# Kernel tuning notes

Hardware: AMD Instinct MI355X
Metric: run time of the kernel (lower is better)

Reference implementation:

```python
import jax, jax.numpy as jnp
import numpy as np

VOCAB, EMB, NDIM, B, T = 50000, 300, 512, 128, 128


def gru_cell(x, h, Wih, Whh, bih, bhh):
    # torch nn.GRU gate order: [r, z, n]
    gi = x @ Wih.T + bih
    gh = h @ Whh.T + bhh
    i_r, i_z, i_n = jnp.split(gi, 3, axis=-1)
    h_r, h_z, h_n = jnp.split(gh, 3, axis=-1)
    r = jax.nn.sigmoid(i_r + h_r)
    z = jax.nn.sigmoid(i_z + h_z)
    n = jnp.tanh(i_n + r * h_n)
    return (1.0 - z) * n + z * h


def masked_gru(X, mask, h0, Wih, Whh, bih, bhh):
    # X: T x B x d, mask: T x B, h0: B x n. Replicates _gru_forward:
    # step-0 output is stored UNmasked (o_tm1 is None), later steps blend.
    h_raw = gru_cell(X[0], h0, Wih, Whh, bih, bhh)
    m0 = mask[0][:, None]
    h = h_raw * m0 + h0 * (1.0 - m0)
    o = h_raw

    def step(carry, inp):
        h, o = carry
        x_t, m_t = inp
        m = m_t[:, None]
        hr = gru_cell(x_t, h, Wih, Whh, bih, bhh)
        h_new = hr * m + h * (1.0 - m)
        o_new = hr * m + o * (1.0 - m)
        return (h_new, o_new), o_new

    (h_f, _), o_rest = jax.lax.scan(step, (h, o), (X[1:], mask[1:]))
    return jnp.concatenate([o[None], o_rest], axis=0), h_f


def rte_forward(premise, hypothesis, E, p_Wih, p_Whh, p_bih, p_bhh,
                h_Wih, h_Whh, h_bih, h_bhh, m_Wih, m_Whh, m_bih, m_bhh,
                W_y, W_h, W_r, W_alpha, out_W, out_b):
    bsz = premise.shape[0]
    n_dim = W_y.shape[0]
    mask_p = (premise != 0).astype(E.dtype).T            # T x B
    mask_h = (hypothesis != 0).astype(E.dtype).T
    enc_p = E[premise].transpose(1, 0, 2)                # T x B x EMB (eval: no dropout)
    enc_h = E[hypothesis].transpose(1, 0, 2)
    h0 = jnp.zeros((bsz, n_dim), dtype=E.dtype)
    o_p, h_n = masked_gru(enc_p, mask_p, h0, p_Wih, p_Whh, p_bih, p_bhh)
    o_h, _ = masked_gru(enc_h, mask_h, h_n, h_Wih, h_Whh, h_bih, h_bhh)

    Y = o_p.transpose(1, 0, 2)                           # B x Tp x n
    Yw = Y @ W_y                                         # hoisted: constant across steps
    maskY = mask_p.T                                     # B x Tp

    def step(r, inp):
        h_t, m_t = inp
        s = h_t @ W_h + r @ W_r                          # B x n
        M = jnp.tanh(Yw + s[:, None, :])                 # B x Tp x n
        alpha = (M @ W_alpha)[..., 0]                    # B x Tp
        alpha = alpha - 1000.0 * (1.0 - maskY)
        alpha = jax.nn.softmax(alpha, axis=-1)
        a = jnp.einsum('bt,btn->bn', alpha, Y)
        m_in = jnp.concatenate([a, h_t], axis=-1)        # B x 2n
        rr = gru_cell(m_in, r, m_Wih, m_Whh, m_bih, m_bhh)
        m = m_t[:, None]
        r_new = rr * m + r * (1.0 - m)
        return r_new, alpha

    r0 = jnp.zeros((bsz, n_dim), dtype=E.dtype)
    r_f, _alpha_vec = jax.lax.scan(step, r0, (o_h, mask_h))
    logits = r_f @ out_W.T + out_b                       # B x 3
    return jax.nn.log_softmax(logits, axis=-1)


def setup_inputs():
    key = jax.random.key(0)
    ks = jax.random.split(key, 22)
    s = 0.05
    def rn(k, sh):
        return jax.random.normal(k, sh, dtype=jnp.float32) * s
    G = 3 * NDIM
    return {
        "premise": jax.random.randint(ks[0], (B, T), 0, VOCAB),
        "hypothesis": jax.random.randint(ks[1], (B, T), 0, VOCAB),
        "E": rn(ks[2], (VOCAB, EMB)),
        "p_Wih": rn(ks[3], (G, EMB)), "p_Whh": rn(ks[4], (G, NDIM)),
        "p_bih": rn(ks[5], (G,)), "p_bhh": rn(ks[6], (G,)),
        "h_Wih": rn(ks[7], (G, EMB)), "h_Whh": rn(ks[8], (G, NDIM)),
        "h_bih": rn(ks[9], (G,)), "h_bhh": rn(ks[10], (G,)),
        "m_Wih": rn(ks[11], (G, 2 * NDIM)), "m_Whh": rn(ks[12], (G, NDIM)),
        "m_bih": rn(ks[13], (G,)), "m_bhh": rn(ks[14], (G,)),
        "W_y": rn(ks[15], (NDIM, NDIM)), "W_h": rn(ks[16], (NDIM, NDIM)),
        "W_r": rn(ks[17], (NDIM, NDIM)), "W_alpha": rn(ks[18], (NDIM, 1)),
        "out_W": rn(ks[19], (3, NDIM)), "out_b": rn(ks[20], (3,)),
    }


def reference(premise, hypothesis, E, p_Wih, p_Whh, p_bih, p_bhh,
              h_Wih, h_Whh, h_bih, h_bhh, m_Wih, m_Whh, m_bih, m_bhh,
              W_y, W_h, W_r, W_alpha, out_W, out_b):
    return rte_forward(premise, hypothesis, E, p_Wih, p_Whh, p_bih, p_bhh,
                       h_Wih, h_Whh, h_bih, h_bhh, m_Wih, m_Whh, m_bih, m_bhh,
                       W_y, W_h, W_r, W_alpha, out_W, out_b)
```

## Files before the change

kernel.cpp:

```cpp
#include <hip/hip_runtime.h>
#include <math.h>

#define B_SZ 128
#define T_SZ 128
#define EMBD 300
#define ND 512
#define G3 1536
#define FPAD 32
#define NFID 128
#define NREP 8

typedef short s16x8 __attribute__((ext_vector_type(8)));
typedef float f32x4 __attribute__((ext_vector_type(4)));
typedef unsigned long long u64;

__device__ __forceinline__ unsigned short f2b(float x) {
    unsigned u = __float_as_uint(x);
    unsigned r = (u + 0x7fff + ((u >> 16) & 1)) >> 16;
    return (unsigned short)r;
}
__device__ __forceinline__ float b2f(unsigned short v) {
    return __uint_as_float(((unsigned)v) << 16);
}
__device__ __forceinline__ float fsigmoid(float x) { return 1.0f / (1.0f + __expf(-x)); }
__device__ __forceinline__ float ftanh(float x) { return 1.0f - 2.0f / (__expf(2.0f * x) + 1.0f); }

__device__ __forceinline__ f32x4 mfma16(s16x8 a, s16x8 b, f32x4 c) {
    return __builtin_amdgcn_mfma_f32_16x16x32_bf16(a, b, c, 0, 0, 0);
}

__device__ __forceinline__ u64 cld64(const void* p) {
    return __hip_atomic_load((const u64*)p, __ATOMIC_RELAXED, __HIP_MEMORY_SCOPE_AGENT);
}
__device__ __forceinline__ void cst64(void* p, u64 v) {
    __hip_atomic_store((u64*)p, v, __ATOMIC_RELAXED, __HIP_MEMORY_SCOPE_AGENT);
}
__device__ __forceinline__ unsigned cld32(const void* p) {
    return __hip_atomic_load((const unsigned*)p, __ATOMIC_RELAXED, __HIP_MEMORY_SCOPE_AGENT);
}
__device__ __forceinline__ void cst32(void* p, unsigned v) {
    __hip_atomic_store((unsigned*)p, v, __ATOMIC_RELAXED, __HIP_MEMORY_SCOPE_AGENT);
}
__device__ __forceinline__ s16x8 cld_frag(const unsigned short* p) {
    union { u64 q[2]; s16x8 v; } u;
    u.q[0] = cld64(p);
    u.q[1] = cld64(p + 4);
    return u.v;
}

__device__ __forceinline__ void postflag(unsigned* flags, int base, int id, unsigned ep)
{
    if (threadIdx.x < NREP)
        cst32(&flags[((long)threadIdx.x * NFID + base + id) * FPAD], ep);
}
__device__ __forceinline__ void waitflags(const unsigned* flags, int base, int n,
                                          unsigned ep, int rep)
{
    const unsigned* fr = flags + (long)rep * NFID * FPAD;
    if (threadIdx.x < 64) {
#pragma unroll 1
        for (int i = threadIdx.x; i < n; i += 64)
            while (cld32(&fr[(long)(base + i) * FPAD]) < ep)
                __builtin_amdgcn_s_sleep(2);
    }
    __syncthreads();
}
__device__ __forceinline__ void fbar(unsigned* flags, int base, int nb, unsigned ep)
{
    __syncthreads();
    postflag(flags, base, blockIdx.x & 63, ep);
    waitflags(flags, base, nb, ep, blockIdx.x & 7);
}

#define FB_GRUP 0
#define FB_GRUH 64

template<typename AT, bool OB>
__global__ __launch_bounds__(256)
void mfma_gemm(const AT* __restrict__ A, const int* __restrict__ idxA,
               const unsigned short* __restrict__ Wb, const float* __restrict__ bias,
               void* __restrict__ Cv,
               int M, int N, int K, int ldA, int Kpad, int ldC)
{
    __shared__ unsigned short As[64][40];
    __shared__ unsigned short Bs[64][40];
    const int tid = threadIdx.x;
    const int wv = tid >> 6, lane = tid & 63;
    const int wm = wv >> 1, wn = wv & 1;
    const int m0 = blockIdx.y * 64, n0 = blockIdx.x * 64;

    f32x4 acc[2][2] = {{{0.f,0.f,0.f,0.f},{0.f,0.f,0.f,0.f}},
                       {{0.f,0.f,0.f,0.f},{0.f,0.f,0.f,0.f}}};
    const int r_st = tid >> 2, k_st = (tid & 3) * 8;

    long arow = -1;
    {
        int gm = m0 + r_st;
        if (gm < M) arow = idxA ? (long)idxA[gm] : (long)gm;
    }

    const int kIters = (K + 31) / 32;
    for (int it = 0; it < kIters; ++it) {
        const int kg = it * 32 + k_st;
        {
            s16x8 pk = {0,0,0,0,0,0,0,0};
            if (arow >= 0) {
                if constexpr (sizeof(AT) == 2) {
                    if (kg + 8 <= K) {
                        pk = *(const s16x8*)((const unsigned short*)A + arow * (long)ldA + kg);
                    } else {
#pragma unroll
                        for (int j = 0; j < 8; ++j)
                            if (kg + j < K) pk[j] = (short)((const unsigned short*)A)[arow * (long)ldA + kg + j];
                    }
                } else {
                    if (kg + 8 <= K) {
                        const float* p = (const float*)A + arow * (long)ldA + kg;
                        f32x4 u0 = *(const f32x4*)p;
                        f32x4 u1 = *(const f32x4*)(p + 4);
#pragma unroll
                        for (int j = 0; j < 4; ++j) { pk[j] = (short)f2b(u0[j]); pk[4+j] = (short)f2b(u1[j]); }
                    } else {
#pragma unroll
                        for (int j = 0; j < 8; ++j) {
                            int kk = kg + j;
                            if (kk < K) pk[j] = (short)f2b(((const float*)A)[arow * (long)ldA + kk]);
                        }
                    }
                }
            }
            *(s16x8*)&As[r_st][k_st] = pk;
        }
        {
            int gn = n0 + r_st;
            s16x8 pk = {0,0,0,0,0,0,0,0};
            if (gn < N) pk = *(const s16x8*)&Wb[(long)gn * Kpad + kg];
            *(s16x8*)&Bs[r_st][k_st] = pk;
        }
        __syncthreads();
        {
            const int koff = (lane >> 4) * 8;
            s16x8 af[2], bfr[2];
#pragma unroll
            for (int f = 0; f < 2; ++f) {
                af[f]  = *(s16x8*)&As[wm * 32 + f * 16 + (lane & 15)][koff];
                bfr[f] = *(s16x8*)&Bs[wn * 32 + f * 16 + (lane & 15)][koff];
            }
#pragma unroll
            for (int fi = 0; fi < 2; ++fi)
#pragma unroll
                for (int fj = 0; fj < 2; ++fj)
                    acc[fi][fj] = mfma16(af[fi], bfr[fj], acc[fi][fj]);
        }
        __syncthreads();
    }
#pragma unroll
    for (int fi = 0; fi < 2; ++fi)
#pragma unroll
        for (int fj = 0; fj < 2; ++fj)
#pragma unroll
            for (int r = 0; r < 4; ++r) {
                int m = m0 + wm * 32 + fi * 16 + (lane >> 4) * 4 + r;
                int n = n0 + wn * 32 + fj * 16 + (lane & 15);
                if (m < M && n < N) {
                    float v = acc[fi][fj][r];
                    if (bias) v += bias[n];
                    if constexpr (OB) ((unsigned short*)Cv)[(long)m * ldC + n] = f2b(v);
                    else               ((float*)Cv)[(long)m * ldC + n] = v;
                }
            }
}

#define GRU_NB 64
__global__ __launch_bounds__(256, 1)
void gru_chain(const unsigned short* __restrict__ Whh_b, const float* __restrict__ GI,
               const float* __restrict__ bhh, const int* __restrict__ toks,
               float* __restrict__ h32,
               unsigned short* __restrict__ h16a, unsigned short* __restrict__ h16b,
               unsigned short* __restrict__ o_bt,
               unsigned* __restrict__ flags, int fbase)
{
    __shared__ unsigned short wlds[3][16][512];
    __shared__ unsigned short ht[64][20];
    const int tid = threadIdx.x;
    const int wv = tid >> 6, lane = tid & 63;
    const int dt = blockIdx.x & 31, bh = blockIdx.x >> 5;
    const int b0 = bh * 64;

    for (int s = 0; s < 12; ++s) {
        int slot = tid + s * 256;
        int g = slot >> 10, rem = slot & 1023, ks = rem >> 6, ln = rem & 63;
        int row = g * ND + dt * 16 + (ln & 15);
        int k = ks * 32 + (ln >> 4) * 8;
        *(s16x8*)&wlds[g][ks][ln * 8] = *(const s16x8*)&Whh_b[(long)row * ND + k];
    }
    __syncthreads();

    const int d = dt * 16 + (lane & 15);
    const int brow = b0 + wv * 16 + (lane >> 4) * 4;
    const long fhrd = ((long)(bh * 4 + wv) * 16) << 9;

    const int bl = tid & 63, dq = tid >> 6;
    const long fhwr = (((long)(bh * 4 + (bl >> 4)) * 16 + (dt >> 1)) << 9)
                    + (((((dt & 1) * 16 + dq * 4) >> 3) * 16 + (bl & 15)) * 8)
                    + (((dt & 1) * 16 + dq * 4) & 7);

    float hreg[4];
#pragma unroll
    for (int rr = 0; rr < 4; ++rr) hreg[rr] = h32[(long)(brow + rr) * ND + d];

    float o_run[4] = {0.f, 0.f, 0.f, 0.f};
    unsigned ep = 0;

    for (int t = 0; t < T_SZ; ++t) {
        const unsigned short* hin16 = (t & 1) ? h16b : h16a;
        unsigned short* hout16 = (t & 1) ? h16a : h16b;

        const float* git = GI + (long)t * (B_SZ * G3);
        float gi_r[4], gi_z[4], gi_n[4]; int mk[4];
#pragma unroll
        for (int rr = 0; rr < 4; ++rr) {
            int b = brow + rr;
            gi_r[rr] = git[(long)b * G3 + d];
            gi_z[rr] = git[(long)b * G3 + ND + d];
            gi_n[rr] = git[(long)b * G3 + 2 * ND + d];
            mk[rr]   = toks[b * T_SZ + t];
        }

        f32x4 acc0 = {0,0,0,0}, acc1 = {0,0,0,0}, acc2 = {0,0,0,0};
#pragma unroll
        for (int ks = 0; ks < 16; ++ks) {
            s16x8 a  = cld_frag(&hin16[fhrd + ((long)ks << 9) + lane * 8]);
            s16x8 br = *(s16x8*)&wlds[0][ks][lane * 8];
            s16x8 bz = *(s16x8*)&wlds[1][ks][lane * 8];
            s16x8 bn = *(s16x8*)&wlds[2][ks][lane * 8];
            acc0 = mfma16(a, br, acc0);
            acc1 = mfma16(a, bz, acc1);
            acc2 = mfma16(a, bn, acc2);
        }

#pragma unroll
        for (int rr = 0; rr < 4; ++rr) {
            int b = brow + rr;
            float rg = fsigmoid(gi_r[rr] + acc0[rr] + bhh[d]);
            float zg = fsigmoid(gi_z[rr] + acc1[rr] + bhh[ND + d]);
            float ng = ftanh(gi_n[rr] + rg * (acc2[rr] + bhh[2 * ND + d]));
            float hr = (1.0f - zg) * ng + zg * hreg[rr];
            bool m = mk[rr] != 0;
            float hn = m ? hr : hreg[rr];
            hreg[rr] = hn;
            ht[b - b0][lane & 15] = f2b(hn);
            if (t == T_SZ - 1) h32[(long)b * ND + d] = hn;
            o_run[rr] = (t == 0) ? hr : (m ? hr : o_run[rr]);
            o_bt[((long)b * T_SZ + t) * ND + d] = f2b(o_run[rr]);
        }
        __syncthreads();
        {
            u64 v = *(u64*)&ht[bl][dq * 4];
            cst64(&hout16[fhwr], v);
        }
        fbar(flags, fbase, GRU_NB, ++ep);
    }
}

__global__ __launch_bounds__(512, 1)
void match_pb(const unsigned short* __restrict__ Ws,
              const unsigned short* __restrict__ Wg,
              const unsigned short* __restrict__ OHWh_bt,
              const unsigned short* __restrict__ OHGI_bt,
              const float* __restrict__ m_bhh, const float* __restrict__ Walpha,
              const unsigned short* __restrict__ Yw_bb,
              const unsigned short* __restrict__ Y_bb,
              const int* __restrict__ prem, const int* __restrict__ hyp,
              float* __restrict__ r32)
{
    __shared__ unsigned short ylds[T_SZ][ND];
    __shared__ float xv[1024];
    __shared__ float sarr[512];
    __shared__ float wal[512];
    __shared__ float part[512];
    __shared__ float lg[T_SZ];

    const int b = blockIdx.x;
    const int tid = threadIdx.x;
    const int tp = tid >> 2, q = tid & 3;

    for (int s = 0; s < 16; ++s) {
        int c = s * 512 + tid;
        int row = c >> 6, cg = c & 63;
        *(s16x8*)&ylds[row][cg * 8] =
            *(const s16x8*)&Y_bb[((long)b * T_SZ + row) * ND + cg * 8];
    }
    s16x8 ywr[16];
#pragma unroll
    for (int i8 = 0; i8 < 16; ++i8)
        ywr[i8] = *(const s16x8*)&Yw_bb[((long)b * T_SZ + tp) * ND + q * 128 + i8 * 8];

    wal[tid] = Walpha[tid];
    xv[512 + tid] = 0.0f;
    float mm = 0.f;
    if (tid < T_SZ) mm = (prem[b * T_SZ + tid] != 0) ? 0.f : 1000.f;
    __syncthreads();

    const float* sp  = &sarr[q * 128];
    const float* wap = &wal[q * 128];

    for (int t = 0; t < T_SZ; ++t) {
        {
            float acc = 0.f;
            const unsigned short* wp = Ws + (long)tid * 8;
#pragma unroll 4
            for (int k8 = 0; k8 < 64; ++k8) {
                f32x4 x0 = *(const f32x4*)&xv[512 + k8 * 8];
                f32x4 x1 = *(const f32x4*)&xv[512 + k8 * 8 + 4];
                s16x8 w = *(const s16x8*)(wp + ((long)k8 << 12));
#pragma unroll
                for (int j = 0; j < 4; ++j) {
                    acc += b2f((unsigned short)w[j]) * x0[j];
                    acc += b2f((unsigned short)w[4 + j]) * x1[j];
                }
            }
            sarr[tid] = acc + b2f(OHWh_bt[((long)b * T_SZ + t) * ND + tid]);
        }
        __syncthreads();
        {
            float acc = 0.f;
#pragma unroll
            for (int i8 = 0; i8 < 16; ++i8) {
                s16x8 yw = ywr[i8];
                f32x4 s0 = *(const f32x4*)&sp[i8 * 8];
                f32x4 s1 = *(const f32x4*)&sp[i8 * 8 + 4];
                f32x4 w0 = *(const f32x4*)&wap[i8 * 8];
                f32x4 w1 = *(const f32x4*)&wap[i8 * 8 + 4];
#pragma unroll
                for (int j = 0; j < 4; ++j)
                    acc += ftanh(b2f((unsigned short)yw[j]) + s0[j]) * w0[j];
#pragma unroll
                for (int j = 0; j < 4; ++j)
                    acc += ftanh(b2f((unsigned short)yw[4 + j]) + s1[j]) * w1[j];
            }
            part[tid] = acc;
        }
        __syncthreads();
        if (tid < T_SZ)
            lg[tid] = __expf(part[tid * 4] + part[tid * 4 + 1]
                           + part[tid * 4 + 2] + part[tid * 4 + 3] - mm);
        __syncthreads();
        {
            float suml = 0.f, av = 0.f;
#pragma unroll 8
            for (int tpp = 0; tpp < T_SZ; ++tpp) {
                float al = lg[tpp];
                suml += al;
                av += al * b2f(ylds[tpp][tid]);
            }
            xv[tid] = av / suml;
        }
        __syncthreads();
        {
            float aR = 0.f, aZ = 0.f, aGN = 0.f, aHN = 0.f;
            const unsigned short* wb = Wg + (long)tid * 8;
#pragma unroll 2
            for (int k8 = 0; k8 < 64; ++k8) {
                f32x4 xa0 = *(const f32x4*)&xv[k8 * 8];
                f32x4 xa1 = *(const f32x4*)&xv[k8 * 8 + 4];
                f32x4 xr0 = *(const f32x4*)&xv[512 + k8 * 8];
                f32x4 xr1 = *(const f32x4*)&xv[512 + k8 * 8 + 4];
                const long ko = (long)k8 << 12;
                s16x8 wRa = *(const s16x8*)(wb + ko);
                s16x8 wZa = *(const s16x8*)(wb + ko + (1L << 18));
                s16x8 wNa = *(const s16x8*)(wb + ko + (2L << 18));
                s16x8 wRr = *(const s16x8*)(wb + ko + (3L << 18));
                s16x8 wZr = *(const s16x8*)(wb + ko + (4L << 18));
                s16x8 wNr = *(const s16x8*)(wb + ko + (5L << 18));
#pragma unroll
                for (int j = 0; j < 4; ++j) {
                    aR  += b2f((unsigned short)wRa[j]) * xa0[j];
                    aR  += b2f((unsigned short)wRa[4 + j]) * xa1[j];
                    aZ  += b2f((unsigned short)wZa[j]) * xa0[j];
                    aZ  += b2f((unsigned short)wZa[4 + j]) * xa1[j];
                    aGN += b2f((unsigned short)wNa[j]) * xa0[j];
                    aGN += b2f((unsigned short)wNa[4 + j]) * xa1[j];
                    aR  += b2f((unsigned short)wRr[j]) * xr0[j];
                    aR  += b2f((unsigned short)wRr[4 + j]) * xr1[j];
                    aZ  += b2f((unsigned short)wZr[j]) * xr0[j];
                    aZ  += b2f((unsigned short)wZr[4 + j]) * xr1[j];
                    aHN += b2f((unsigned short)wNr[j]) * xr0[j];
                    aHN += b2f((unsigned short)wNr[4 + j]) * xr1[j];
                }
            }
            const unsigned short* og = OHGI_bt + ((long)b * T_SZ + t) * G3;
            float rg = fsigmoid(aR + b2f(og[tid]) + m_bhh[tid]);
            float zg = fsigmoid(aZ + b2f(og[ND + tid]) + m_bhh[ND + tid]);
            float ng = ftanh(aGN + b2f(og[2 * ND + tid])
                             + rg * (aHN + m_bhh[2 * ND + tid]));
            float rp = xv[512 + tid];
            float rn = (1.0f - zg) * ng + zg * rp;
            bool mk = hyp[b * T_SZ + t] != 0;
            float v = mk ? rn : rp;
            __syncthreads();
            xv[512 + tid] = v;
        }
        __syncthreads();
    }
    r32[(long)b * ND + tid] = xv[512 + tid];
}

__global__ void prep_idx(const int* __restrict__ prem, const int* __restrict__ hyp,
                         int* __restrict__ idx_p, int* __restrict__ idx_h)
{
    int i = blockIdx.x * blockDim.x + threadIdx.x;
    if (i < B_SZ * T_SZ) {
        int t = i / B_SZ, b = i % B_SZ;
        idx_p[i] = prem[b * T_SZ + t];
        idx_h[i] = hyp[b * T_SZ + t];
    }
}

__global__ void conv_w(const float* __restrict__ in, unsigned short* __restrict__ out,
                       int N, int K, int Kpad, int ldIn, int colOff)
{
    long i = (long)blockIdx.x * blockDim.x + threadIdx.x;
    if (i >= (long)N * Kpad) return;
    int n = (int)(i / Kpad), k = (int)(i % Kpad);
    float v = (k < K) ? in[(long)n * ldIn + k + colOff] : 0.0f;
    out[i] = f2b(v);
}

__global__ void conv_wT(const float* __restrict__ in, unsigned short* __restrict__ out,
                        int N, int K, int Kpad, int ldIn)
{
    long i = (long)blockIdx.x * blockDim.x + threadIdx.x;
    if (i >= (long)N * Kpad) return;
    int n = (int)(i / Kpad), k = (int)(i % Kpad);
    float v = (k < K) ? in[(long)k * ldIn + n] : 0.0f;
    out[i] = f2b(v);
}

__global__ void pack_ws(const float* __restrict__ Wr, unsigned short* __restrict__ out)
{
    long i = (long)blockIdx.x * blockDim.x + threadIdx.x;
    if (i >= 64L * 512 * 8) return;
    int k8 = (int)(i >> 12), n = (int)((i >> 3) & 511), j = (int)(i & 7);
    out[i] = f2b(Wr[(long)(k8 * 8 + j) * ND + n]);
}

__global__ void pack_wg(const float* __restrict__ mWih, const float* __restrict__ mWhh,
                        unsigned short* __restrict__ out)
{
    long i = (long)blockIdx.x * blockDim.x + threadIdx.x;
    if (i >= 6L * 64 * 512 * 8) return;
    int fam = (int)(i >> 18);
    long rem = i & 262143;
    int k8 = (int)(rem >> 12), n = (int)((rem >> 3) & 511), j = (int)(rem & 7);
    int k = k8 * 8 + j;
    float v;
    if (fam < 3) v = mWih[(long)(fam * ND + n) * 1024 + k];
    else         v = mWhh[(long)((fam - 3) * ND + n) * ND + k];
    out[i] = f2b(v);
}

__global__ void zero_kernel(float* __restrict__ p, int n)
{
    int i = blockIdx.x * blockDim.x + threadIdx.x;
    if (i < n) p[i] = 0.0f;
}

__global__ void final_logits(const float* __restrict__ r, const float* __restrict__ outW,
                             const float* __restrict__ outb, float* __restrict__ out)
{
    int b = blockIdx.x;
    int lane = threadIdx.x;
    float a0 = 0.0f, a1 = 0.0f, a2 = 0.0f;
    for (int k = lane; k < ND; k += 64) {
        float rv = r[(long)b * ND + k];
        a0 += rv * outW[0 * ND + k];
        a1 += rv * outW[1 * ND + k];
        a2 += rv * outW[2 * ND + k];
    }
#pragma unroll
    for (int off = 32; off; off >>= 1) {
        a0 += __shfl_down(a0, off);
        a1 += __shfl_down(a1, off);
        a2 += __shfl_down(a2, off);
    }
    if (lane == 0) {
        float l0 = a0 + outb[0], l1 = a1 + outb[1], l2 = a2 + outb[2];
        float mx = fmaxf(l0, fmaxf(l1, l2));
        float se = expf(l0 - mx) + expf(l1 - mx) + expf(l2 - mx);
        float ls = mx + logf(se);
        out[b * 3 + 0] = l0 - ls;
        out[b * 3 + 1] = l1 - ls;
        out[b * 3 + 2] = l2 - ls;
    }
}

extern "C" void kernel_launch(void* const* d_in, const int* in_sizes, int n_in,
                              void* d_out, int out_size, void* d_ws, size_t ws_size,
                              hipStream_t stream)
{
    const int*   prem    = (const int*)d_in[0];
    const int*   hyp     = (const int*)d_in[1];
    const float* E       = (const float*)d_in[2];
    const float* p_Wih   = (const float*)d_in[3];
    const float* p_Whh   = (const float*)d_in[4];
    const float* p_bih   = (const float*)d_in[5];
    const float* p_bhh   = (const float*)d_in[6];
    const float* h_Wih   = (const float*)d_in[7];
    const float* h_Whh   = (const float*)d_in[8];
    const float* h_bih   = (const float*)d_in[9];
    const float* h_bhh   = (const float*)d_in[10];
    const float* m_Wih   = (const float*)d_in[11];
    const float* m_Whh   = (const float*)d_in[12];
    const float* m_bih   = (const float*)d_in[13];
    const float* m_bhh   = (const float*)d_in[14];
    const float* W_y     = (const float*)d_in[15];
    const float* W_h     = (const float*)d_in[16];
    const float* W_r     = (const float*)d_in[17];
    const float* W_alpha = (const float*)d_in[18];
    const float* out_W   = (const float*)d_in[19];
    const float* out_b   = (const float*)d_in[20];
    float* out = (float*)d_out;

    const int MB = T_SZ * B_SZ;
    const int NFLAGS = NREP * NFID * FPAD;

    float* ws = (float*)d_ws;
    size_t off = 0;
    float* GI    = ws + off; off += (size_t)MB * G3;
    float* h32   = ws + off; off += (size_t)B_SZ * ND;
    float* r32   = ws + off; off += (size_t)B_SZ * ND;
    unsigned* flags = (unsigned*)(ws + off); off += NFLAGS;
    int* idx_p = (int*)(ws + off); off += (size_t)B_SZ * T_SZ;
    int* idx_h = (int*)(ws + off); off += (size_t)B_SZ * T_SZ;
    unsigned short* ub = (unsigned short*)(ws + off);
    size_t uoff = 0;
    unsigned short* o_p_bt = ub + uoff; uoff += (size_t)MB * ND;
    unsigned short* o_h_bt = ub + uoff; uoff += (size_t)MB * ND;
    unsigned short* Yw_bb  = ub + uoff; uoff += (size_t)MB * ND;
    unsigned short* OHWh_bt= ub + uoff; uoff += (size_t)MB * ND;
    unsigned short* OHGI_bt= ub + uoff; uoff += (size_t)MB * G3;
    unsigned short* h16a   = ub + uoff; uoff += (size_t)B_SZ * ND;
    unsigned short* h16b   = ub + uoff; uoff += (size_t)B_SZ * ND;
    unsigned short* pWih_b = ub + uoff; uoff += (size_t)G3 * 320;
    unsigned short* hWih_b = ub + uoff; uoff += (size_t)G3 * 320;
    unsigned short* pWhh_b = ub + uoff; uoff += (size_t)G3 * ND;
    unsigned short* hWhh_b = ub + uoff; uoff += (size_t)G3 * ND;
    unsigned short* mWihR  = ub + uoff; uoff += (size_t)G3 * ND;
    unsigned short* WyT_b  = ub + uoff; uoff += (size_t)ND * ND;
    unsigned short* WhT_b  = ub + uoff; uoff += (size_t)ND * ND;
    unsigned short* Ws_p   = ub + uoff; uoff += 64L * 512 * 8;
    unsigned short* Wg_p   = ub + uoff; uoff += 6L * 64 * 512 * 8;
    off += (uoff + 1) / 2;
    if (ws_size < off * sizeof(float)) return;

    auto cblk = [](long n) { return (int)((n + 255) / 256); };

    prep_idx<<<cblk(MB), 256, 0, stream>>>(prem, hyp, idx_p, idx_h);
    conv_w <<<cblk((long)G3 * 320), 256, 0, stream>>>(p_Wih, pWih_b, G3, EMBD, 320, EMBD, 0);
    conv_w <<<cblk((long)G3 * 320), 256, 0, stream>>>(h_Wih, hWih_b, G3, EMBD, 320, EMBD, 0);
    conv_w <<<cblk((long)G3 * ND), 256, 0, stream>>>(p_Whh, pWhh_b, G3, ND, ND, ND, 0);
    conv_w <<<cblk((long)G3 * ND), 256, 0, stream>>>(h_Whh, hWhh_b, G3, ND, ND, ND, 0);
    conv_w <<<cblk((long)G3 * ND), 256, 0, stream>>>(m_Wih, mWihR, G3, ND, ND, 2 * ND, ND);
    conv_wT<<<cblk((long)ND * ND), 256, 0, stream>>>(W_y, WyT_b, ND, ND, ND, ND);
    conv_wT<<<cblk((long)ND * ND), 256, 0, stream>>>(W_h, WhT_b, ND, ND, ND, ND);
    pack_ws<<<cblk(64L * 512 * 8), 256, 0, stream>>>(W_r, Ws_p);
    pack_wg<<<cblk(6L * 64 * 512 * 8), 256, 0, stream>>>(m_Wih, m_Whh, Wg_p);
    zero_kernel<<<cblk(B_SZ * ND), 256, 0, stream>>>(h32, B_SZ * ND);
    zero_kernel<<<cblk(B_SZ * ND / 2), 256, 0, stream>>>((float*)h16a, B_SZ * ND / 2);
    zero_kernel<<<cblk(NFLAGS), 256, 0, stream>>>((float*)flags, NFLAGS);

    {
        dim3 g(G3 / 64, MB / 64);
        mfma_gemm<float, false><<<g, 256, 0, stream>>>(E, idx_p, pWih_b, p_bih, GI,
                                                       MB, G3, EMBD, EMBD, 320, G3);
    }
    gru_chain<<<GRU_NB, 256, 0, stream>>>(pWhh_b, GI, p_bhh, prem, h32, h16a, h16b,
                                          o_p_bt, flags, FB_GRUP);

    {
        dim3 g(G3 / 64, MB / 64);
        mfma_gemm<float, false><<<g, 256, 0, stream>>>(E, idx_h, hWih_b, h_bih, GI,
                                                       MB, G3, EMBD, EMBD, 320, G3);
    }
    gru_chain<<<GRU_NB, 256, 0, stream>>>(hWhh_b, GI, h_bhh, hyp, h32, h16a, h16b,
                                          o_h_bt, flags, FB_GRUH);

    {
        dim3 g(ND / 64, MB / 64);
        mfma_gemm<unsigned short, true><<<g, 256, 0, stream>>>(o_p_bt, nullptr, WyT_b, nullptr,
                                                               Yw_bb, MB, ND, ND, ND, ND, ND);
        mfma_gemm<unsigned short, true><<<g, 256, 0, stream>>>(o_h_bt, nullptr, WhT_b, nullptr,
                                                               OHWh_bt, MB, ND, ND, ND, ND, ND);
        dim3 g2(G3 / 64, MB / 64);
        mfma_gemm<unsigned short, true><<<g2, 256, 0, stream>>>(o_h_bt, nullptr, mWihR, m_bih,
                                                                OHGI_bt, MB, G3, ND, ND, ND, G3);
    }

    match_pb<<<B_SZ, 512, 0, stream>>>(Ws_p, Wg_p, OHWh_bt, OHGI_bt, m_bhh, W_alpha,
                                       Yw_bb, o_p_bt, prem, hyp, r32);

    final_logits<<<B_SZ, 64, 0, stream>>>(r32, out_W, out_b, out);
}
```

Baseline: 7.689 ms.

## Use packed bf16 v_dot2 in match kernel with bf16-packed activations

Rewrites the match_pb recurrence to use v_dot2_f32_bf16 for the Ws and Wg matvecs and for the attention-weighted sum over Y. Activations (attention context, recurrent state, softmax weights) are packed to bf16 pairs in shared memory, and Y is stored as interleaved time-pairs so each dot2 covers two timesteps. This halves the multiply-add instruction count and removes per-element bf16-to-float unpacking, but adds extra pack steps and barriers per timestep and rounds activations and softmax weights to bf16, which loses precision.

```diff
diff --git a/kernel.cpp b/kernel.cpp
--- a/kernel.cpp
+++ b/kernel.cpp
@@ -22,8 +22,16 @@
 __device__ __forceinline__ float b2f(unsigned short v) {
     return __uint_as_float(((unsigned)v) << 16);
 }
+__device__ __forceinline__ unsigned pk2(float lo, float hi) {
+    return (unsigned)f2b(lo) | ((unsigned)f2b(hi) << 16);
+}
 __device__ __forceinline__ float fsigmoid(float x) { return 1.0f / (1.0f + __expf(-x)); }
 __device__ __forceinline__ float ftanh(float x) { return 1.0f - 2.0f / (__expf(2.0f * x) + 1.0f); }
+
+__device__ __forceinline__ float dot2bf(unsigned a, unsigned b, float c) {
+    asm("v_dot2_f32_bf16 %0, %1, %2, %0" : "+v"(c) : "v"(a), "v"(b));
+    return c;
+}
 
 __device__ __forceinline__ f32x4 mfma16(s16x8 a, s16x8 b, f32x4 c) {
     return __builtin_amdgcn_mfma_f32_16x16x32_bf16(a, b, c, 0, 0, 0);
@@ -274,22 +282,29 @@
               const int* __restrict__ prem, const int* __restrict__ hyp,
               float* __restrict__ r32)
 {
-    __shared__ unsigned short ylds[T_SZ][ND];
-    __shared__ float xv[1024];
+    __shared__ unsigned ytp[64][512];
     __shared__ float sarr[512];
     __shared__ float wal[512];
     __shared__ float part[512];
     __shared__ float lg[T_SZ];
+    __shared__ unsigned lgp[64];
+    __shared__ unsigned xa16[256];
+    __shared__ unsigned xr16[256];
+    __shared__ float xr32[512];
 
     const int b = blockIdx.x;
     const int tid = threadIdx.x;
     const int tp = tid >> 2, q = tid & 3;
 
-    for (int s = 0; s < 16; ++s) {
-        int c = s * 512 + tid;
-        int row = c >> 6, cg = c & 63;
-        *(s16x8*)&ylds[row][cg * 8] =
-            *(const s16x8*)&Y_bb[((long)b * T_SZ + row) * ND + cg * 8];
+    for (int s = 0; s < 8; ++s) {
+        int idx = s * 512 + tid;
+        int rp = idx >> 6, n0 = (idx & 63) * 8;
+        s16x8 y0 = *(const s16x8*)&Y_bb[((long)b * T_SZ + 2 * rp) * ND + n0];
+        s16x8 y1 = *(const s16x8*)&Y_bb[((long)b * T_SZ + 2 * rp + 1) * ND + n0];
+#pragma unroll
+        for (int j = 0; j < 8; ++j)
+            ytp[rp][n0 + j] = (unsigned)(unsigned short)y0[j]
+                            | ((unsigned)(unsigned short)y1[j] << 16);
     }
     s16x8 ywr[16];
 #pragma unroll
@@ -297,28 +312,30 @@
         ywr[i8] = *(const s16x8*)&Yw_bb[((long)b * T_SZ + tp) * ND + q * 128 + i8 * 8];
 
     wal[tid] = Walpha[tid];
-    xv[512 + tid] = 0.0f;
+    xr32[tid] = 0.0f;
+    if (tid < 256) xr16[tid] = 0u;
     float mm = 0.f;
     if (tid < T_SZ) mm = (prem[b * T_SZ + tid] != 0) ? 0.f : 1000.f;
     __syncthreads();
 
     const float* sp  = &sarr[q * 128];
     const float* wap = &wal[q * 128];
+    const unsigned* wsp = (const unsigned*)Ws + tid * 4;
+    const unsigned* wgp = (const unsigned*)Wg + tid * 4;
+    const unsigned ONE2 = 0x3F803F80u;
 
     for (int t = 0; t < T_SZ; ++t) {
         {
             float acc = 0.f;
-            const unsigned short* wp = Ws + (long)tid * 8;
 #pragma unroll 4
             for (int k8 = 0; k8 < 64; ++k8) {
-                f32x4 x0 = *(const f32x4*)&xv[512 + k8 * 8];
-                f32x4 x1 = *(const f32x4*)&xv[512 + k8 * 8 + 4];
-                s16x8 w = *(const s16x8*)(wp + ((long)k8 << 12));
-#pragma unroll
-                for (int j = 0; j < 4; ++j) {
-                    acc += b2f((unsigned short)w[j]) * x0[j];
-                    acc += b2f((unsigned short)w[4 + j]) * x1[j];
-                }
+                unsigned x0 = xr16[k8 * 4], x1 = xr16[k8 * 4 + 1];
+                unsigned x2 = xr16[k8 * 4 + 2], x3 = xr16[k8 * 4 + 3];
+                const unsigned* w = wsp + (long)k8 * 2048;
+                acc = dot2bf(w[0], x0, acc);
+                acc = dot2bf(w[1], x1, acc);
+                acc = dot2bf(w[2], x2, acc);
+                acc = dot2bf(w[3], x3, acc);
             }
             sarr[tid] = acc + b2f(OHWh_bt[((long)b * T_SZ + t) * ND + tid]);
         }
@@ -346,64 +363,67 @@
             lg[tid] = __expf(part[tid * 4] + part[tid * 4 + 1]
                            + part[tid * 4 + 2] + part[tid * 4 + 3] - mm);
         __syncthreads();
-        {
-            float suml = 0.f, av = 0.f;
+        if (tid < 64) lgp[tid] = pk2(lg[2 * tid], lg[2 * tid + 1]);
+        __syncthreads();
+        {
+            float av = 0.f, su = 0.f;
 #pragma unroll 8
-            for (int tpp = 0; tpp < T_SZ; ++tpp) {
-                float al = lg[tpp];
-                suml += al;
-                av += al * b2f(ylds[tpp][tid]);
+            for (int i = 0; i < 64; ++i) {
+                unsigned l2 = lgp[i];
+                unsigned y2 = ytp[i][tid];
+                av = dot2bf(l2, y2, av);
+                su = dot2bf(l2, ONE2, su);
             }
-            xv[tid] = av / suml;
-        }
+            part[tid] = av / su;
+        }
+        __syncthreads();
+        if (tid < 256) xa16[tid] = pk2(part[2 * tid], part[2 * tid + 1]);
         __syncthreads();
         {
             float aR = 0.f, aZ = 0.f, aGN = 0.f, aHN = 0.f;
-            const unsigned short* wb = Wg + (long)tid * 8;
 #pragma unroll 2
             for (int k8 = 0; k8 < 64; ++k8) {
-                f32x4 xa0 = *(const f32x4*)&xv[k8 * 8];
-                f32x4 xa1 = *(const f32x4*)&xv[k8 * 8 + 4];
-                f32x4 xr0 = *(const f32x4*)&xv[512 + k8 * 8];
-                f32x4 xr1 = *(const f32x4*)&xv[512 + k8 * 8 + 4];
-                const long ko = (long)k8 << 12;
-                s16x8 wRa = *(const s16x8*)(wb + ko);
-                s16x8 wZa = *(const s16x8*)(wb + ko + (1L << 18));
-                s16x8 wNa = *(const s16x8*)(wb + ko + (2L << 18));
-                s16x8 wRr = *(const s16x8*)(wb + ko + (3L << 18));
-                s16x8 wZr = *(const s16x8*)(wb + ko + (4L << 18));
-                s16x8 wNr = *(const s16x8*)(wb + ko + (5L << 18));
-#pragma unroll
-                for (int j = 0; j < 4; ++j) {
-                    aR  += b2f((unsigned short)wRa[j]) * xa0[j];
-                    aR  += b2f((unsigned short)wRa[4 + j]) * xa1[j];
-                    aZ  += b2f((unsigned short)wZa[j]) * xa0[j];
-                    aZ  += b2f((unsigned short)wZa[4 + j]) * xa1[j];
-                    aGN += b2f((unsigned short)wNa[j]) * xa0[j];
-                    aGN += b2f((unsigned short)wNa[4 + j]) * xa1[j];
-                    aR  += b2f((unsigned short)wRr[j]) * xr0[j];
-                    aR  += b2f((unsigned short)wRr[4 + j]) * xr1[j];
-                    aZ  += b2f((unsigned short)wZr[j]) * xr0[j];
-                    aZ  += b2f((unsigned short)wZr[4 + j]) * xr1[j];
-                    aHN += b2f((unsigned short)wNr[j]) * xr0[j];
-                    aHN += b2f((unsigned short)wNr[4 + j]) * xr1[j];
-                }
+                unsigned xa0 = xa16[k8 * 4], xa1 = xa16[k8 * 4 + 1];
+                unsigned xa2 = xa16[k8 * 4 + 2], xa3 = xa16[k8 * 4 + 3];
+                unsigned xr0 = xr16[k8 * 4], xr1 = xr16[k8 * 4 + 1];
+                unsigned xr2 = xr16[k8 * 4 + 2], xr3 = xr16[k8 * 4 + 3];
+                const unsigned* w0 = wgp + (long)k8 * 2048;
+                const unsigned* w1 = w0 + (1L << 17);
+                const unsigned* w2 = w0 + (2L << 17);
+                const unsigned* w3 = w0 + (3L << 17);
+                const unsigned* w4 = w0 + (4L << 17);
+                const unsigned* w5 = w0 + (5L << 17);
+                aR  = dot2bf(w0[0], xa0, aR);  aR  = dot2bf(w0[1], xa1, aR);
+                aR  = dot2bf(w0[2], xa2, aR);  aR  = dot2bf(w0[3], xa3, aR);
+                aZ  = dot2bf(w1[0], xa0, aZ);  aZ  = dot2bf(w1[1], xa1, aZ);
+                aZ  = dot2bf(w1[2], xa2, aZ);  aZ  = dot2bf(w1[3], xa3, aZ);
+                aGN = dot2bf(w2[0], xa0, aGN); aGN = dot2bf(w2[1], xa1, aGN);
+                aGN = dot2bf(w2[2], xa2, aGN); aGN = dot2bf(w2[3], xa3, aGN);
+                aR  = dot2bf(w3[0], xr0, aR);  aR  = dot2bf(w3[1], xr1, aR);
+                aR  = dot2bf(w3[2], xr2, aR);  aR  = dot2bf(w3[3], xr3, aR);
+                aZ  = dot2bf(w4[0], xr0, aZ);  aZ  = dot2bf(w4[1], xr1, aZ);
+                aZ  = dot2bf(w4[2], xr2, aZ);  aZ  = dot2bf(w4[3], xr3, aZ);
+                aHN = dot2bf(w5[0], xr0, aHN); aHN = dot2bf(w5[1], xr1, aHN);
+                aHN = dot2bf(w5[2], xr2, aHN); aHN = dot2bf(w5[3], xr3, aHN);
             }
             const unsigned short* og = OHGI_bt + ((long)b * T_SZ + t) * G3;
             float rg = fsigmoid(aR + b2f(og[tid]) + m_bhh[tid]);
             float zg = fsigmoid(aZ + b2f(og[ND + tid]) + m_bhh[ND + tid]);
             float ng = ftanh(aGN + b2f(og[2 * ND + tid])
                              + rg * (aHN + m_bhh[2 * ND + tid]));
-            float rp = xv[512 + tid];
+            float rp = xr32[tid];
             float rn = (1.0f - zg) * ng + zg * rp;
             bool mk = hyp[b * T_SZ + t] != 0;
             float v = mk ? rn : rp;
             __syncthreads();
-            xv[512 + tid] = v;
-        }
-        __syncthreads();
-    }
-    r32[(long)b * ND + tid] = xv[512 + tid];
+            xr32[tid] = v;
+            part[tid] = v;
+        }
+        __syncthreads();
+        if (tid < 256) xr16[tid] = pk2(part[2 * tid], part[2 * tid + 1]);
+        __syncthreads();
+    }
+    r32[(long)b * ND + tid] = xr32[tid];
 }
 
 __global__ void prep_idx(const int* __restrict__ prem, const int* __restrict__ hyp,
```

New measurement: 7.502 ms. 2.4% less time.
